# Kernel optimization log

Measured on AMD Instinct MI355X. Metric: run time of the kernel, lower is better.

Reference implementation:

```python
import jax, jax.numpy as jnp
import numpy as np

B, S, E = 2, 2048, 2048
H, KV, D = 16, 4, 128
G = H // KV
ROPE_THETA = 10000.0


def setup_inputs() -> dict:
    key = jax.random.key(0)
    ks = jax.random.split(key, 8)
    std = 0.02
    return {
        "x": jax.random.normal(ks[0], (B, S, E), jnp.float32),
        "Wq": jax.random.normal(ks[1], (H * D, E), jnp.float32) * std,
        "bq": jax.random.normal(ks[2], (H * D,), jnp.float32) * std,
        "Wk": jax.random.normal(ks[3], (KV * D, E), jnp.float32) * std,
        "bk": jax.random.normal(ks[4], (KV * D,), jnp.float32) * std,
        "Wv": jax.random.normal(ks[5], (KV * D, E), jnp.float32) * std,
        "bv": jax.random.normal(ks[6], (KV * D,), jnp.float32) * std,
        "Wo": jax.random.normal(ks[7], (E, H * D), jnp.float32) * std,
    }


def _rope_cos_sin(seq_len, head_dim):
    inv_freq = 1.0 / (ROPE_THETA ** (jnp.arange(0, head_dim, 2, dtype=jnp.float32) / head_dim))
    pos = jnp.arange(seq_len, dtype=jnp.float32)  # rope scale factor = 1.0
    freqs = pos[:, None] * inv_freq[None, :]        # [S, D/2]
    emb = jnp.concatenate([freqs, freqs], axis=-1)  # [S, D]
    return jnp.cos(emb), jnp.sin(emb)


def _apply_rope(t, cos, sin):
    # t: [..., S, <extra dims>, D]; cos/sin: [S, D] broadcast over extra dims
    half = t.shape[-1] // 2
    extra = t.ndim - 3  # dims between S (axis 1) and D (last)
    c = cos.reshape((1, cos.shape[0]) + (1,) * extra + (cos.shape[1],))
    s = sin.reshape((1, sin.shape[0]) + (1,) * extra + (sin.shape[1],))
    rot = jnp.concatenate([-t[..., half:], t[..., :half]], axis=-1)
    return t * c + rot * s


def reference(x, Wq, bq, Wk, bk, Wv, bv, Wo):
    b, s, e = x.shape
    # QKV projections (biases on q/k/v, none on o)
    q = (jnp.einsum("bse,he->bsh", x, Wq) + bq).reshape(b, s, KV, G, D)
    k = (jnp.einsum("bse,he->bsh", x, Wk) + bk).reshape(b, s, KV, D)
    v = (jnp.einsum("bse,he->bsh", x, Wv) + bv).reshape(b, s, KV, D)

    cos, sin = _rope_cos_sin(s, D)
    q = _apply_rope(q, cos, sin)
    k = _apply_rope(k, cos, sin)

    scale = 1.0 / jnp.sqrt(jnp.float32(D))
    # GQA: q heads grouped per kv head; k/v broadcast over group dim
    scores = jnp.einsum("bskgd,btkd->bkgst", q, k) * scale  # [B,KV,G,S,S]
    causal = jnp.tril(jnp.ones((s, s), dtype=bool))
    scores = jnp.where(causal, scores, jnp.float32(-1e9))
    attn = jax.nn.softmax(scores, axis=-1)
    out = jnp.einsum("bkgst,btkd->bskgd", attn, v).reshape(b, s, H * D)
    return jnp.einsum("bsh,eh->bse", out, Wo)
```

## Files before the change

kernel.cpp:

```cpp
#include <hip/hip_runtime.h>
#include <hip/hip_bf16.h>
#include <math.h>

#define BB 2
#define SS 2048
#define EE 2048
#define HH 16
#define KVH 4
#define DD 128
#define QTILES 32

typedef short short8 __attribute__((ext_vector_type(8)));
typedef float f32x4 __attribute__((ext_vector_type(4)));

__device__ __forceinline__ unsigned int f2bf1(float x) {
    union { float f; unsigned int u; } v; v.f = x;
    return (v.u + 0x7FFFu + ((v.u >> 16) & 1u)) >> 16;
}
__device__ __forceinline__ unsigned int packbf(float a, float b) {
    return f2bf1(a) | (f2bf1(b) << 16);
}
__device__ __forceinline__ void gl_lds16(const void* g, void* l) {
    __builtin_amdgcn_global_load_lds(
        (const __attribute__((address_space(1))) unsigned int*)g,
        (__attribute__((address_space(3))) unsigned int*)l,
        16, 0, 0);
}

__global__ __launch_bounds__(256) void cvt_all_kernel(
    const float* __restrict__ x,  const float* __restrict__ Wq,
    const float* __restrict__ Wk, const float* __restrict__ Wv,
    const float* __restrict__ Wo, const float* __restrict__ bq,
    const float* __restrict__ bk, const float* __restrict__ bv,
    unsigned short* __restrict__ xb, unsigned short* __restrict__ wqkv,
    unsigned short* __restrict__ wob, float* __restrict__ bqkv)
{
    long id = (long)blockIdx.x * 256 + threadIdx.x;
    const float* src; unsigned short* dst; long j;
    if (id < 2097152)      { j = id;           src = x;  dst = xb; }
    else if (id < 3145728) { j = id - 2097152; src = Wq; dst = wqkv; }
    else if (id < 3407872) { j = id - 3145728; src = Wk; dst = wqkv + 4194304; }
    else if (id < 3670016) { j = id - 3407872; src = Wv; dst = wqkv + 5242880; }
    else if (id < 4718592) { j = id - 3670016; src = Wo; dst = wob; }
    else if (id < 4719360) {
        long c = (id - 4718592) * 4;
#pragma unroll
        for (int e = 0; e < 4; ++e) {
            long cc = c + e;
            bqkv[cc] = (cc < 2048) ? bq[cc] : (cc < 2560 ? bk[cc - 2048] : bv[cc - 2560]);
        }
        return;
    } else return;
    float4 f = ((const float4*)src)[j];
    ((uint2*)dst)[j] = make_uint2(packbf(f.x, f.y), packbf(f.z, f.w));
}

template <bool OUT_BF16>
__global__ __launch_bounds__(256) void gemm_mfma_kernel(
    const unsigned short* __restrict__ A, const unsigned short* __restrict__ W,
    const float* __restrict__ bias, void* __restrict__ Cout,
    int M, int N, int K)
{
    __shared__ unsigned short As[128 * 32];
    __shared__ unsigned short Bs[128 * 32];

    const int tid  = threadIdx.x;
    const int w    = tid >> 6;
    const int lane = tid & 63;
    const int quad = lane >> 4;
    const int l16  = lane & 15;
    const int wr   = w >> 1, wc = w & 1;
    const int m0 = blockIdx.y * 128, n0 = blockIdx.x * 128;

    f32x4 acc[4][4];
#pragma unroll
    for (int i = 0; i < 4; ++i)
#pragma unroll
        for (int j = 0; j < 4; ++j) acc[i][j] = (f32x4){0.f, 0.f, 0.f, 0.f};

    const unsigned short* Ag = A + (size_t)(m0 + w * 32 + (lane >> 2)) * K + (lane & 3) * 8;
    const unsigned short* Wg = W + (size_t)(n0 + w * 32 + (lane >> 2)) * K + (lane & 3) * 8;
    unsigned short* AsB = &As[(w * 32) * 32];
    unsigned short* BsB = &Bs[(w * 32) * 32];

    for (int k0 = 0; k0 < K; k0 += 32) {
        gl_lds16(Ag + k0, AsB);
        gl_lds16(Ag + k0 + (size_t)16 * K, AsB + 16 * 32);
        gl_lds16(Wg + k0, BsB);
        gl_lds16(Wg + k0 + (size_t)16 * K, BsB + 16 * 32);
        __syncthreads();

        short8 a_f[4], b_f[4];
#pragma unroll
        for (int i = 0; i < 4; ++i)
            a_f[i] = *(const short8*)&As[(wr * 64 + i * 16 + l16) * 32 + quad * 8];
#pragma unroll
        for (int j = 0; j < 4; ++j)
            b_f[j] = *(const short8*)&Bs[(wc * 64 + j * 16 + l16) * 32 + quad * 8];
#pragma unroll
        for (int i = 0; i < 4; ++i)
#pragma unroll
            for (int j = 0; j < 4; ++j)
                acc[i][j] = __builtin_amdgcn_mfma_f32_16x16x32_bf16(a_f[i], b_f[j], acc[i][j], 0, 0, 0);
        __syncthreads();
    }

    float bj[4];
#pragma unroll
    for (int j = 0; j < 4; ++j)
        bj[j] = bias ? bias[n0 + wc * 64 + j * 16 + l16] : 0.0f;
#pragma unroll
    for (int i = 0; i < 4; ++i) {
#pragma unroll
        for (int r = 0; r < 4; ++r) {
            size_t row = m0 + wr * 64 + i * 16 + quad * 4 + r;
#pragma unroll
            for (int j = 0; j < 4; ++j) {
                size_t col = n0 + wc * 64 + j * 16 + l16;
                float val = acc[i][j][r] + bj[j];
                if (OUT_BF16)
                    ((unsigned short*)Cout)[row * N + col] = (unsigned short)f2bf1(val);
                else
                    ((float*)Cout)[row * N + col] = val;
            }
        }
    }
}

__global__ __launch_bounds__(64) void rope_kernel(unsigned short* __restrict__ qkv)
{
    int bix = blockIdx.x;
    int m, col;
    if (bix < 65536) { m = bix >> 4; col = (bix & 15) * 128; }
    else { int i = bix - 65536; m = i >> 2; col = 2048 + (i & 3) * 128; }
    int s = m & (SS - 1);
    int d = threadIdx.x;
    unsigned short* p = qkv + (size_t)m * 3072 + col;
    float inv_freq = expf(-(float)d * (logf(10000.0f) / 64.0f));
    float fr = (float)s * inv_freq;
    float c = cosf(fr), sn = sinf(fr);
    union { unsigned int u; float f; } x1, x2;
    x1.u = ((unsigned int)p[d]) << 16;
    x2.u = ((unsigned int)p[d + 64]) << 16;
    p[d]      = (unsigned short)f2bf1(x1.f * c - x2.f * sn);
    p[d + 64] = (unsigned short)f2bf1(x2.f * c + x1.f * sn);
}

__global__ __launch_bounds__(256, 2) void attn_mfma_kernel(
    const unsigned short* __restrict__ qkv, unsigned short* __restrict__ o)
{
    __shared__ unsigned int Ks_u[2][64 * 64];
    __shared__ unsigned int Vs_u[2][128 * 32];
    __shared__ unsigned short Ps[4][16 * 64];

    const int tid  = threadIdx.x;
    const int w    = tid >> 6;
    const int lane = tid & 63;
    const int quad = lane >> 4;
    const int l16  = lane & 15;
    const int jpair = blockIdx.x;
    const int h     = blockIdx.y;
    const int b     = blockIdx.z;
    const int kv    = h >> 2;

    const float k2 = 0.12752789744920764f;

    const unsigned short* kbase = qkv + (size_t)b * SS * 3072 + 2048 + kv * 128;
    const unsigned short* vbase = kbase + 512;

    const int kc  = tid & 15;
    const int kp0 = tid >> 4;
    const int vpp = tid >> 3;
    const int vd0 = (tid & 7) * 16;

    for (int pass = 0; pass < 2; ++pass) {
        const int qt = pass ? (QTILES - 1 - jpair) : jpair;
        const int q0 = qt * 64;

        short8 qf[4];
        {
            const unsigned short* qp = qkv + (size_t)(b * SS + q0 + w * 16 + l16) * 3072 + h * 128 + quad * 8;
#pragma unroll
            for (int ks = 0; ks < 4; ++ks)
                qf[ks] = *(const short8*)(qp + ks * 32);
        }

        uint4 kpre[4], vpa[2], vpb[2];
        {
            const unsigned short* kg = kbase + (size_t)kp0 * 3072 + kc * 8;
#pragma unroll
            for (int rr = 0; rr < 4; ++rr)
                kpre[rr] = *(const uint4*)(kg + (size_t)rr * 16 * 3072);
            const unsigned short* vg = vbase + (size_t)(2 * vpp) * 3072 + vd0;
            vpa[0] = *(const uint4*)(vg);
            vpa[1] = *(const uint4*)(vg + 8);
            vpb[0] = *(const uint4*)(vg + 3072);
            vpb[1] = *(const uint4*)(vg + 3072 + 8);
        }

        float m_r[4], l_r[4];
        f32x4 Oacc[8];
#pragma unroll
        for (int r = 0; r < 4; ++r) { m_r[r] = -1e30f; l_r[r] = 0.0f; }
#pragma unroll
        for (int ot = 0; ot < 8; ++ot) Oacc[ot] = (f32x4){0.f, 0.f, 0.f, 0.f};

        for (int t = 0; t <= qt; ++t) {
            const int buf = t & 1;
            unsigned int* Kb = Ks_u[buf];
            unsigned int* Vb = Vs_u[buf];

#pragma unroll
            for (int rr = 0; rr < 4; ++rr) {
                int pos = kp0 + rr * 16;
                int key = (kp0 + rr) & 7;
                *(uint4*)&Kb[pos * 64 + (kc ^ key) * 4] = kpre[rr];
            }
            {
                const unsigned int* pa = (const unsigned int*)vpa;
                const unsigned int* pb = (const unsigned int*)vpb;
#pragma unroll
                for (int j = 0; j < 8; ++j) {
                    unsigned lo = __builtin_amdgcn_perm(pb[j], pa[j], 0x05040100);
                    unsigned hi = __builtin_amdgcn_perm(pb[j], pa[j], 0x07060302);
                    int d0 = vd0 + 2 * j;
                    int g  = d0 >> 4;
                    int k0 = (d0 + g) & 7;
                    int k1 = (d0 + 1 + g) & 7;
                    Vb[d0 * 32 + (((vpp >> 2) ^ k0) & 7) * 4 + (vpp & 3)] = lo;
                    Vb[(d0 + 1) * 32 + (((vpp >> 2) ^ k1) & 7) * 4 + (vpp & 3)] = hi;
                }
            }

            if (t < qt) {
                const unsigned short* kg = kbase + (size_t)((t + 1) * 64 + kp0) * 3072 + kc * 8;
#pragma unroll
                for (int rr = 0; rr < 4; ++rr)
                    kpre[rr] = *(const uint4*)(kg + (size_t)rr * 16 * 3072);
                const unsigned short* vg = vbase + (size_t)((t + 1) * 64 + 2 * vpp) * 3072 + vd0;
                vpa[0] = *(const uint4*)(vg);
                vpa[1] = *(const uint4*)(vg + 8);
                vpb[0] = *(const uint4*)(vg + 3072);
                vpb[1] = *(const uint4*)(vg + 3072 + 8);
            }
            __syncthreads();

            f32x4 S[4];
#pragma unroll
            for (int ct = 0; ct < 4; ++ct) {
                f32x4 s = (f32x4){0.f, 0.f, 0.f, 0.f};
                const int row = ct * 16 + l16;
                const int key = (l16 + ct) & 7;
#pragma unroll
                for (int ks = 0; ks < 4; ++ks) {
                    short8 kf = *(const short8*)&Kb[row * 64 + ((ks * 4 + quad) ^ key) * 4];
                    s = __builtin_amdgcn_mfma_f32_16x16x32_bf16(qf[ks], kf, s, 0, 0, 0);
                }
                S[ct] = s;
            }

            if (t == qt) {
                const int rowloc = w * 16 + quad * 4;
#pragma unroll
                for (int ct = 0; ct < 4; ++ct)
#pragma unroll
                    for (int r = 0; r < 4; ++r)
                        if (ct * 16 + l16 > rowloc + r) S[ct][r] = -1e30f;
            }

#pragma unroll
            for (int r = 0; r < 4; ++r) {
                float c0 = fmaxf(fmaxf(S[0][r], S[1][r]), fmaxf(S[2][r], S[3][r]));
                c0 = fmaxf(c0, __shfl_xor(c0, 1));
                c0 = fmaxf(c0, __shfl_xor(c0, 2));
                c0 = fmaxf(c0, __shfl_xor(c0, 4));
                c0 = fmaxf(c0, __shfl_xor(c0, 8));
                float mnew = fmaxf(m_r[r], c0);
                float alpha = exp2f((m_r[r] - mnew) * k2);
                m_r[r] = mnew;
                float mh = mnew * k2;
                float rs = 0.0f;
                const int prow = quad * 4 + r;
                const int pkey = (prow >> 2) ^ ((prow & 3) << 1);
#pragma unroll
                for (int ct = 0; ct < 4; ++ct) {
                    float p = exp2f(S[ct][r] * k2 - mh);
                    rs += p;
                    int chunk = ct * 2 + (l16 >> 3);
                    union { float f; unsigned u; } pu; pu.f = p;
                    Ps[w][prow * 64 + (chunk ^ pkey) * 8 + (l16 & 7)] =
                        (unsigned short)((pu.u + 0x8000u) >> 16);
                }
                rs += __shfl_xor(rs, 1);
                rs += __shfl_xor(rs, 2);
                rs += __shfl_xor(rs, 4);
                rs += __shfl_xor(rs, 8);
                l_r[r] = l_r[r] * alpha + rs;
#pragma unroll
                for (int ot = 0; ot < 8; ++ot) Oacc[ot][r] *= alpha;
            }

            {
                const int pkeyr = (l16 >> 2) ^ ((l16 & 3) << 1);
                short8 pf0 = *(const short8*)&Ps[w][l16 * 64 + (quad ^ pkeyr) * 8];
                short8 pf1 = *(const short8*)&Ps[w][l16 * 64 + ((4 + quad) ^ pkeyr) * 8];
#pragma unroll
                for (int ot = 0; ot < 8; ++ot) {
                    const int d = ot * 16 + l16;
                    const int vkey = (l16 + ot) & 7;
                    short8 v0 = *(const short8*)&Vb[d * 32 + (quad ^ vkey) * 4];
                    Oacc[ot] = __builtin_amdgcn_mfma_f32_16x16x32_bf16(pf0, v0, Oacc[ot], 0, 0, 0);
                    short8 v1 = *(const short8*)&Vb[d * 32 + ((4 + quad) ^ vkey) * 4];
                    Oacc[ot] = __builtin_amdgcn_mfma_f32_16x16x32_bf16(pf1, v1, Oacc[ot], 0, 0, 0);
                }
            }
        }

        float inv[4];
#pragma unroll
        for (int r = 0; r < 4; ++r) inv[r] = 1.0f / l_r[r];
        const int orow0 = q0 + w * 16 + quad * 4;
        unsigned short* ob = o + (size_t)(b * SS + orow0) * 2048 + h * 128 + l16;
#pragma unroll
        for (int r = 0; r < 4; ++r)
#pragma unroll
            for (int ot = 0; ot < 8; ++ot)
                ob[(size_t)r * 2048 + ot * 16] = (unsigned short)f2bf1(Oacc[ot][r] * inv[r]);

        __syncthreads();
    }
}

extern "C" void kernel_launch(void* const* d_in, const int* in_sizes, int n_in,
                              void* d_out, int out_size, void* d_ws, size_t ws_size,
                              hipStream_t stream)
{
    const float* x  = (const float*)d_in[0];
    const float* Wq = (const float*)d_in[1];
    const float* bq = (const float*)d_in[2];
    const float* Wk = (const float*)d_in[3];
    const float* bk = (const float*)d_in[4];
    const float* Wv = (const float*)d_in[5];
    const float* bv = (const float*)d_in[6];
    const float* Wo = (const float*)d_in[7];
    float* out = (float*)d_out;

    const int M = BB * SS;
    char* wsb = (char*)d_ws;
    unsigned short* xb   = (unsigned short*)wsb;  wsb += (size_t)M * EE * 2;
    unsigned short* wqkv = (unsigned short*)wsb;  wsb += (size_t)3072 * EE * 2;
    unsigned short* wob  = (unsigned short*)wsb;  wsb += (size_t)EE * EE * 2;
    unsigned short* qkvb = (unsigned short*)wsb;  wsb += (size_t)M * 3072 * 2;
    unsigned short* abb  = (unsigned short*)wsb;  wsb += (size_t)M * 2048 * 2;
    float* bqkv = (float*)wsb;

    cvt_all_kernel<<<18435, 256, 0, stream>>>(x, Wq, Wk, Wv, Wo, bq, bk, bv,
                                              xb, wqkv, wob, bqkv);

    gemm_mfma_kernel<true><<<dim3(3072 / 128, M / 128), 256, 0, stream>>>(
        xb, wqkv, bqkv, qkvb, M, 3072, EE);

    rope_kernel<<<M * HH + M * KVH, 64, 0, stream>>>(qkvb);

    attn_mfma_kernel<<<dim3(16, HH, BB), 256, 0, stream>>>(qkvb, abb);

    gemm_mfma_kernel<false><<<dim3(EE / 128, M / 128), 256, 0, stream>>>(
        abb, wob, nullptr, out, M, EE, 2048);
}
```

Measured before the change: 376.3 us.

## Use 128-row query tiles per block with single-buffered K/V and DPP reductions

The attention kernel now has each block handle one 128-row query tile, with each wave owning 32 rows as two 16-row sub-tiles. This replaces the previous scheme of two 64-row passes paired for causal balance, and each K/V tile loaded into LDS now feeds twice as many MFMAs. K/V LDS goes from double-buffered to single-buffered with an extra barrier per iteration, row max/sum reductions use DPP instead of shuffles, and output is staged through LDS for 16-byte coalesced stores. The grid must shrink to 16 q-tiles, and the launch code for that is not shown. Causal load balance changes and register pressure rises.

New measurement: 425.0 us. 12.9% more time.

```diff
diff --git a/kernel.cpp b/kernel.cpp
--- a/kernel.cpp
+++ b/kernel.cpp
@@ -8,7 +8,6 @@
 #define HH 16
 #define KVH 4
 #define DD 128
-#define QTILES 32
 
 typedef short short8 __attribute__((ext_vector_type(8)));
 typedef float f32x4 __attribute__((ext_vector_type(4)));
@@ -25,6 +24,23 @@
         (const __attribute__((address_space(1))) unsigned int*)g,
         (__attribute__((address_space(3))) unsigned int*)l,
         16, 0, 0);
+}
+
+#define DPPF(x, ctrl) __int_as_float(__builtin_amdgcn_update_dpp( \
+    0, __float_as_int(x), ctrl, 0xf, 0xf, true))
+__device__ __forceinline__ float rmax16(float x) {
+    x = fmaxf(x, DPPF(x, 0xB1));
+    x = fmaxf(x, DPPF(x, 0x4E));
+    x = fmaxf(x, DPPF(x, 0x141));
+    x = fmaxf(x, DPPF(x, 0x140));
+    return x;
+}
+__device__ __forceinline__ float rsum16(float x) {
+    x += DPPF(x, 0xB1);
+    x += DPPF(x, 0x4E);
+    x += DPPF(x, 0x141);
+    x += DPPF(x, 0x140);
+    return x;
 }
 
 __global__ __launch_bounds__(256) void cvt_all_kernel(
@@ -149,21 +165,23 @@
 __global__ __launch_bounds__(256, 2) void attn_mfma_kernel(
     const unsigned short* __restrict__ qkv, unsigned short* __restrict__ o)
 {
-    __shared__ unsigned int Ks_u[2][64 * 64];
-    __shared__ unsigned int Vs_u[2][128 * 32];
-    __shared__ unsigned short Ps[4][16 * 64];
+    __shared__ unsigned int Ks_u[64 * 64];
+    __shared__ unsigned int Vs_u[128 * 32];
+    __shared__ unsigned short Ps[4][32 * 64];
 
     const int tid  = threadIdx.x;
     const int w    = tid >> 6;
     const int lane = tid & 63;
     const int quad = lane >> 4;
     const int l16  = lane & 15;
-    const int jpair = blockIdx.x;
-    const int h     = blockIdx.y;
-    const int b     = blockIdx.z;
-    const int kv    = h >> 2;
+    const int qt   = 15 - blockIdx.x;
+    const int h    = blockIdx.y;
+    const int b    = blockIdx.z;
+    const int kv   = h >> 2;
 
     const float k2 = 0.12752789744920764f;
+    const int q0 = qt * 128;
+    const int nt = 2 * qt + 2;
 
     const unsigned short* kbase = qkv + (size_t)b * SS * 3072 + 2048 + kv * 128;
     const unsigned short* vbase = kbase + 512;
@@ -173,115 +191,122 @@
     const int vpp = tid >> 3;
     const int vd0 = (tid & 7) * 16;
 
-    for (int pass = 0; pass < 2; ++pass) {
-        const int qt = pass ? (QTILES - 1 - jpair) : jpair;
-        const int q0 = qt * 64;
-
-        short8 qf[4];
+    short8 qf[2][4];
+#pragma unroll
+    for (int s = 0; s < 2; ++s) {
+        const unsigned short* qp =
+            qkv + (size_t)(b * SS + q0 + w * 32 + s * 16 + l16) * 3072 + h * 128 + quad * 8;
+#pragma unroll
+        for (int ks = 0; ks < 4; ++ks)
+            qf[s][ks] = *(const short8*)(qp + ks * 32);
+    }
+
+    uint4 kpre[4], vpa[2], vpb[2];
+    {
+        const unsigned short* kg = kbase + (size_t)kp0 * 3072 + kc * 8;
+#pragma unroll
+        for (int rr = 0; rr < 4; ++rr)
+            kpre[rr] = *(const uint4*)(kg + (size_t)rr * 16 * 3072);
+        const unsigned short* vg = vbase + (size_t)(2 * vpp) * 3072 + vd0;
+        vpa[0] = *(const uint4*)(vg);
+        vpa[1] = *(const uint4*)(vg + 8);
+        vpb[0] = *(const uint4*)(vg + 3072);
+        vpb[1] = *(const uint4*)(vg + 3072 + 8);
+    }
+
+    float m_r[2][4], l_r[2][4];
+    f32x4 Oacc[2][8];
+#pragma unroll
+    for (int s = 0; s < 2; ++s)
+#pragma unroll
+        for (int r = 0; r < 4; ++r) { m_r[s][r] = -1e30f; l_r[s][r] = 0.0f; }
+#pragma unroll
+    for (int s = 0; s < 2; ++s)
+#pragma unroll
+        for (int ot = 0; ot < 8; ++ot) Oacc[s][ot] = (f32x4){0.f, 0.f, 0.f, 0.f};
+
+    for (int t = 0; t < nt; ++t) {
+        if (t) __syncthreads();
+
+#pragma unroll
+        for (int rr = 0; rr < 4; ++rr) {
+            int pos = kp0 + rr * 16;
+            int key = (kp0 + rr) & 7;
+            *(uint4*)&Ks_u[pos * 64 + (kc ^ key) * 4] = kpre[rr];
+        }
         {
-            const unsigned short* qp = qkv + (size_t)(b * SS + q0 + w * 16 + l16) * 3072 + h * 128 + quad * 8;
-#pragma unroll
-            for (int ks = 0; ks < 4; ++ks)
-                qf[ks] = *(const short8*)(qp + ks * 32);
-        }
-
-        uint4 kpre[4], vpa[2], vpb[2];
-        {
-            const unsigned short* kg = kbase + (size_t)kp0 * 3072 + kc * 8;
+            const unsigned int* pa = (const unsigned int*)vpa;
+            const unsigned int* pb = (const unsigned int*)vpb;
+#pragma unroll
+            for (int j = 0; j < 8; ++j) {
+                unsigned lo = __builtin_amdgcn_perm(pb[j], pa[j], 0x05040100);
+                unsigned hi = __builtin_amdgcn_perm(pb[j], pa[j], 0x07060302);
+                int d0 = vd0 + 2 * j;
+                int g  = d0 >> 4;
+                int k0 = (d0 + g) & 7;
+                int k1 = (d0 + 1 + g) & 7;
+                Vs_u[d0 * 32 + (((vpp >> 2) ^ k0) & 7) * 4 + (vpp & 3)] = lo;
+                Vs_u[(d0 + 1) * 32 + (((vpp >> 2) ^ k1) & 7) * 4 + (vpp & 3)] = hi;
+            }
+        }
+        __syncthreads();
+
+        if (t + 1 < nt) {
+            const unsigned short* kg = kbase + (size_t)((t + 1) * 64 + kp0) * 3072 + kc * 8;
 #pragma unroll
             for (int rr = 0; rr < 4; ++rr)
                 kpre[rr] = *(const uint4*)(kg + (size_t)rr * 16 * 3072);
-            const unsigned short* vg = vbase + (size_t)(2 * vpp) * 3072 + vd0;
+            const unsigned short* vg = vbase + (size_t)((t + 1) * 64 + 2 * vpp) * 3072 + vd0;
             vpa[0] = *(const uint4*)(vg);
             vpa[1] = *(const uint4*)(vg + 8);
             vpb[0] = *(const uint4*)(vg + 3072);
             vpb[1] = *(const uint4*)(vg + 3072 + 8);
         }
 
-        float m_r[4], l_r[4];
-        f32x4 Oacc[8];
-#pragma unroll
-        for (int r = 0; r < 4; ++r) { m_r[r] = -1e30f; l_r[r] = 0.0f; }
-#pragma unroll
-        for (int ot = 0; ot < 8; ++ot) Oacc[ot] = (f32x4){0.f, 0.f, 0.f, 0.f};
-
-        for (int t = 0; t <= qt; ++t) {
-            const int buf = t & 1;
-            unsigned int* Kb = Ks_u[buf];
-            unsigned int* Vb = Vs_u[buf];
-
-#pragma unroll
-            for (int rr = 0; rr < 4; ++rr) {
-                int pos = kp0 + rr * 16;
-                int key = (kp0 + rr) & 7;
-                *(uint4*)&Kb[pos * 64 + (kc ^ key) * 4] = kpre[rr];
-            }
-            {
-                const unsigned int* pa = (const unsigned int*)vpa;
-                const unsigned int* pb = (const unsigned int*)vpb;
-#pragma unroll
-                for (int j = 0; j < 8; ++j) {
-                    unsigned lo = __builtin_amdgcn_perm(pb[j], pa[j], 0x05040100);
-                    unsigned hi = __builtin_amdgcn_perm(pb[j], pa[j], 0x07060302);
-                    int d0 = vd0 + 2 * j;
-                    int g  = d0 >> 4;
-                    int k0 = (d0 + g) & 7;
-                    int k1 = (d0 + 1 + g) & 7;
-                    Vb[d0 * 32 + (((vpp >> 2) ^ k0) & 7) * 4 + (vpp & 3)] = lo;
-                    Vb[(d0 + 1) * 32 + (((vpp >> 2) ^ k1) & 7) * 4 + (vpp & 3)] = hi;
+        f32x4 S0[4], S1[4];
+#pragma unroll
+        for (int ct = 0; ct < 4; ++ct) {
+            f32x4 s0 = (f32x4){0.f, 0.f, 0.f, 0.f};
+            f32x4 s1 = (f32x4){0.f, 0.f, 0.f, 0.f};
+            const int row = ct * 16 + l16;
+            const int key = (l16 + ct) & 7;
+#pragma unroll
+            for (int ks = 0; ks < 4; ++ks) {
+                short8 kf = *(const short8*)&Ks_u[row * 64 + ((ks * 4 + quad) ^ key) * 4];
+                s0 = __builtin_amdgcn_mfma_f32_16x16x32_bf16(qf[0][ks], kf, s0, 0, 0, 0);
+                s1 = __builtin_amdgcn_mfma_f32_16x16x32_bf16(qf[1][ks], kf, s1, 0, 0, 0);
+            }
+            S0[ct] = s0; S1[ct] = s1;
+        }
+
+        if (t >= nt - 2) {
+            const int p0 = t * 64;
+            const int rw = q0 + w * 32 + quad * 4;
+#pragma unroll
+            for (int ct = 0; ct < 4; ++ct) {
+                const int col = p0 + ct * 16 + l16;
+#pragma unroll
+                for (int r = 0; r < 4; ++r) {
+                    if (col > rw + r)      S0[ct][r] = -1e30f;
+                    if (col > rw + 16 + r) S1[ct][r] = -1e30f;
                 }
             }
-
-            if (t < qt) {
-                const unsigned short* kg = kbase + (size_t)((t + 1) * 64 + kp0) * 3072 + kc * 8;
-#pragma unroll
-                for (int rr = 0; rr < 4; ++rr)
-                    kpre[rr] = *(const uint4*)(kg + (size_t)rr * 16 * 3072);
-                const unsigned short* vg = vbase + (size_t)((t + 1) * 64 + 2 * vpp) * 3072 + vd0;
-                vpa[0] = *(const uint4*)(vg);
-                vpa[1] = *(const uint4*)(vg + 8);
-                vpb[0] = *(const uint4*)(vg + 3072);
-                vpb[1] = *(const uint4*)(vg + 3072 + 8);
-            }
-            __syncthreads();
-
-            f32x4 S[4];
-#pragma unroll
-            for (int ct = 0; ct < 4; ++ct) {
-                f32x4 s = (f32x4){0.f, 0.f, 0.f, 0.f};
-                const int row = ct * 16 + l16;
-                const int key = (l16 + ct) & 7;
-#pragma unroll
-                for (int ks = 0; ks < 4; ++ks) {
-                    short8 kf = *(const short8*)&Kb[row * 64 + ((ks * 4 + quad) ^ key) * 4];
-                    s = __builtin_amdgcn_mfma_f32_16x16x32_bf16(qf[ks], kf, s, 0, 0, 0);
-                }
-                S[ct] = s;
-            }
-
-            if (t == qt) {
-                const int rowloc = w * 16 + quad * 4;
-#pragma unroll
-                for (int ct = 0; ct < 4; ++ct)
-#pragma unroll
-                    for (int r = 0; r < 4; ++r)
-                        if (ct * 16 + l16 > rowloc + r) S[ct][r] = -1e30f;
-            }
-
+        }
+
+#pragma unroll
+        for (int s = 0; s < 2; ++s) {
+            f32x4* S = s ? S1 : S0;
 #pragma unroll
             for (int r = 0; r < 4; ++r) {
                 float c0 = fmaxf(fmaxf(S[0][r], S[1][r]), fmaxf(S[2][r], S[3][r]));
-                c0 = fmaxf(c0, __shfl_xor(c0, 1));
-                c0 = fmaxf(c0, __shfl_xor(c0, 2));
-                c0 = fmaxf(c0, __shfl_xor(c0, 4));
-                c0 = fmaxf(c0, __shfl_xor(c0, 8));
-                float mnew = fmaxf(m_r[r], c0);
-                float alpha = exp2f((m_r[r] - mnew) * k2);
-                m_r[r] = mnew;
+                c0 = rmax16(c0);
+                float mnew = fmaxf(m_r[s][r], c0);
+                float alpha = exp2f((m_r[s][r] - mnew) * k2);
+                m_r[s][r] = mnew;
                 float mh = mnew * k2;
                 float rs = 0.0f;
-                const int prow = quad * 4 + r;
-                const int pkey = (prow >> 2) ^ ((prow & 3) << 1);
+                const int prow = s * 16 + quad * 4 + r;
+                const int pkey = prow & 7;
 #pragma unroll
                 for (int ct = 0; ct < 4; ++ct) {
                     float p = exp2f(S[ct][r] * k2 - mh);
@@ -291,43 +316,58 @@
                     Ps[w][prow * 64 + (chunk ^ pkey) * 8 + (l16 & 7)] =
                         (unsigned short)((pu.u + 0x8000u) >> 16);
                 }
-                rs += __shfl_xor(rs, 1);
-                rs += __shfl_xor(rs, 2);
-                rs += __shfl_xor(rs, 4);
-                rs += __shfl_xor(rs, 8);
-                l_r[r] = l_r[r] * alpha + rs;
-#pragma unroll
-                for (int ot = 0; ot < 8; ++ot) Oacc[ot][r] *= alpha;
-            }
-
-            {
-                const int pkeyr = (l16 >> 2) ^ ((l16 & 3) << 1);
-                short8 pf0 = *(const short8*)&Ps[w][l16 * 64 + (quad ^ pkeyr) * 8];
-                short8 pf1 = *(const short8*)&Ps[w][l16 * 64 + ((4 + quad) ^ pkeyr) * 8];
-#pragma unroll
-                for (int ot = 0; ot < 8; ++ot) {
-                    const int d = ot * 16 + l16;
-                    const int vkey = (l16 + ot) & 7;
-                    short8 v0 = *(const short8*)&Vb[d * 32 + (quad ^ vkey) * 4];
-                    Oacc[ot] = __builtin_amdgcn_mfma_f32_16x16x32_bf16(pf0, v0, Oacc[ot], 0, 0, 0);
-                    short8 v1 = *(const short8*)&Vb[d * 32 + ((4 + quad) ^ vkey) * 4];
-                    Oacc[ot] = __builtin_amdgcn_mfma_f32_16x16x32_bf16(pf1, v1, Oacc[ot], 0, 0, 0);
-                }
-            }
-        }
-
+                rs = rsum16(rs);
+                l_r[s][r] = l_r[s][r] * alpha + rs;
+#pragma unroll
+                for (int ot = 0; ot < 8; ++ot) Oacc[s][ot][r] *= alpha;
+            }
+        }
+
+        {
+            const int pk = l16 & 7;
+            short8 pf00 = *(const short8*)&Ps[w][(l16)      * 64 + ((quad)     ^ pk) * 8];
+            short8 pf01 = *(const short8*)&Ps[w][(l16)      * 64 + ((4 + quad) ^ pk) * 8];
+            short8 pf10 = *(const short8*)&Ps[w][(16 + l16) * 64 + ((quad)     ^ pk) * 8];
+            short8 pf11 = *(const short8*)&Ps[w][(16 + l16) * 64 + ((4 + quad) ^ pk) * 8];
+#pragma unroll
+            for (int ot = 0; ot < 8; ++ot) {
+                const int d = ot * 16 + l16;
+                const int vkey = (l16 + ot) & 7;
+                short8 v0 = *(const short8*)&Vs_u[d * 32 + ((quad) ^ vkey) * 4];
+                Oacc[0][ot] = __builtin_amdgcn_mfma_f32_16x16x32_bf16(pf00, v0, Oacc[0][ot], 0, 0, 0);
+                Oacc[1][ot] = __builtin_amdgcn_mfma_f32_16x16x32_bf16(pf10, v0, Oacc[1][ot], 0, 0, 0);
+                short8 v1 = *(const short8*)&Vs_u[d * 32 + ((4 + quad) ^ vkey) * 4];
+                Oacc[0][ot] = __builtin_amdgcn_mfma_f32_16x16x32_bf16(pf01, v1, Oacc[0][ot], 0, 0, 0);
+                Oacc[1][ot] = __builtin_amdgcn_mfma_f32_16x16x32_bf16(pf11, v1, Oacc[1][ot], 0, 0, 0);
+            }
+        }
+    }
+
+#pragma unroll
+    for (int s = 0; s < 2; ++s) {
         float inv[4];
 #pragma unroll
-        for (int r = 0; r < 4; ++r) inv[r] = 1.0f / l_r[r];
-        const int orow0 = q0 + w * 16 + quad * 4;
-        unsigned short* ob = o + (size_t)(b * SS + orow0) * 2048 + h * 128 + l16;
-#pragma unroll
-        for (int r = 0; r < 4; ++r)
-#pragma unroll
-            for (int ot = 0; ot < 8; ++ot)
-                ob[(size_t)r * 2048 + ot * 16] = (unsigned short)f2bf1(Oacc[ot][r] * inv[r]);
-
-        __syncthreads();
+        for (int r = 0; r < 4; ++r) inv[r] = 1.0f / l_r[s][r];
+#pragma unroll
+        for (int r = 0; r < 4; ++r) {
+            const int row = quad * 4 + r;
+#pragma unroll
+            for (int ot = 0; ot < 8; ot += 2) {
+                unsigned pv = packbf(Oacc[s][ot][r] * inv[r], 0.0f) |
+                              (packbf(Oacc[s][ot + 1][r] * inv[r], 0.0f) << 16);
+                Ps[w][row * 128 + ot * 16 + l16]       = (unsigned short)(pv & 0xffffu);
+                Ps[w][row * 128 + (ot + 1) * 16 + l16] = (unsigned short)(pv >> 16);
+            }
+        }
+#pragma unroll
+        for (int i = 0; i < 4; ++i) {
+            const int row = i * 4 + quad;
+            uint4 val = *(const uint4*)&Ps[w][row * 128 + l16 * 8];
+            unsigned short* op =
+                o + (size_t)(b * SS + q0 + w * 32 + s * 16 + row) * 2048 + h * 128 + l16 * 8;
+            *(uint4*)op = val;
+        }
+        if (s == 0) __builtin_amdgcn_s_waitcnt(0);
     }
 }
 
```
